# Performance work log

Measured on AMD Instinct MI355X. Metric: run time of the kernel, lower is better.

## Reference

```python
import jax, jax.numpy as jnp
import numpy as np

B, N, D, H, HD, FF, E, V, HID = 32, 125, 256, 8, 32, 1024, 5, 32000, 128
S = N + 3
MAXPOS = 512
EPS = 1e-12       # BERT LayerNorm eps
THRESH = 0.7


def setup_inputs() -> dict:
    key = jax.random.key(0)
    ks = iter(jax.random.split(key, 32))
    def rn(shape):
        return jax.random.normal(next(ks), shape, jnp.float32)
    def p(shape):
        return rn(shape) * 0.02
    inp = {
        "h_t": rn((B, D)),
        "e_task": rn((B, D)),
        "e_layout": rn((B, D)),
        "token_embeds": rn((B, N, D)),
        # router: Linear(768,128) -> ReLU -> Linear(128,5)
        "router_W1": p((3 * D, HID)), "router_b1": jnp.zeros((HID,), jnp.float32),
        "router_W2": p((HID, E)), "router_b2": jnp.zeros((E,), jnp.float32),
        "hint_W": p((D, E)), "hint_b": jnp.zeros((E,), jnp.float32),
        # per-expert BERT params, stacked over expert dim E
        "pos_emb": p((E, MAXPOS, D)),
        "type_emb": p((E, D)),                    # token_type_id=0 row only
        "ln_emb_g": jnp.ones((E, D), jnp.float32), "ln_emb_b": jnp.zeros((E, D), jnp.float32),
        "Wq": p((E, D, D)), "bq": jnp.zeros((E, D), jnp.float32),
        "Wk": p((E, D, D)), "bk": jnp.zeros((E, D), jnp.float32),
        "Wv": p((E, D, D)), "bv": jnp.zeros((E, D), jnp.float32),
        "Wo": p((E, D, D)), "bo": jnp.zeros((E, D), jnp.float32),
        "ln_attn_g": jnp.ones((E, D), jnp.float32), "ln_attn_b": jnp.zeros((E, D), jnp.float32),
        "Wf1": p((E, D, FF)), "bf1": jnp.zeros((E, FF), jnp.float32),
        "Wf2": p((E, FF, D)), "bf2": jnp.zeros((E, D), jnp.float32),
        "ln_ffn_g": jnp.ones((E, D), jnp.float32), "ln_ffn_b": jnp.zeros((E, D), jnp.float32),
        "head_W": p((D, V)), "head_b": jnp.zeros((V,), jnp.float32),
        "top_k": 2,
    }
    return inp


def _ln(x, g, b):
    m = jnp.mean(x, axis=-1, keepdims=True)
    v = jnp.mean(jnp.square(x - m), axis=-1, keepdims=True)
    return (x - m) * jax.lax.rsqrt(v + EPS) * g + b


def _expert(pos, typ, g0, b0, Wq, bq, Wk, bk, Wv, bv, Wo, bo, g1, b1,
            Wf1, bf1, Wf2, bf2, g2, b2, x):
    # 1-layer BERT encoder (eval mode, no causal mask for inputs_embeds).
    Bx, Sx, _ = x.shape
    h = _ln(x + pos[:Sx][None] + typ[None, None], g0, b0)        # [B,S,D]
    q = (h @ Wq + bq).reshape(Bx, Sx, H, HD)
    k = (h @ Wk + bk).reshape(Bx, Sx, H, HD)
    v = (h @ Wv + bv).reshape(Bx, Sx, H, HD)
    scores = jnp.einsum("bqhd,bkhd->bhqk", q, k) / np.float32(np.sqrt(HD))
    attn = jax.nn.softmax(scores, axis=-1)
    ctx = jnp.einsum("bhqk,bkhd->bqhd", attn, v).reshape(Bx, Sx, D)
    h = _ln(h + ctx @ Wo + bo, g1, b1)
    f = jax.nn.gelu(h @ Wf1 + bf1, approximate=False)
    h = _ln(h + f @ Wf2 + bf2, g2, b2)
    return h


def reference(h_t, e_task, e_layout, token_embeds,
              router_W1, router_b1, router_W2, router_b2, hint_W, hint_b,
              pos_emb, type_emb, ln_emb_g, ln_emb_b,
              Wq, bq, Wk, bk, Wv, bv, Wo, bo, ln_attn_g, ln_attn_b,
              Wf1, bf1, Wf2, bf2, ln_ffn_g, ln_ffn_b,
              head_W, head_b, top_k):
    prefix = jnp.stack([h_t, e_task, e_layout], axis=1)            # [B,3,D]
    x_t = jnp.concatenate([prefix, token_embeds], axis=1)          # [B,S,D]
    flat = jnp.concatenate([h_t, e_task, e_layout], axis=-1)       # [B,3D]
    gate_logits = (jax.nn.relu(flat @ router_W1 + router_b1) @ router_W2
                   + router_b2 + e_layout @ hint_W + hint_b)
    gate_probs = jax.nn.softmax(gate_logits, axis=-1)              # [B,E]
    topk_vals, topk_idx = jax.lax.top_k(gate_probs, top_k)         # [B,k]
    # k collapses to 1 only if EVERY row's max prob exceeds threshold
    use_k1 = jnp.all(jnp.max(gate_probs, axis=-1) > THRESH)
    keep = jnp.where(jnp.arange(top_k) == 0, 1.0,
                     jnp.where(use_k1, 0.0, 1.0)).astype(gate_probs.dtype)
    w = topk_vals * keep[None, :]                                  # [B,k]
    # run all experts densely (E=5 small), then gated combine
    expert_outs = jax.vmap(_expert, in_axes=(0,) * 20 + (None,))(
        pos_emb, type_emb, ln_emb_g, ln_emb_b,
        Wq, bq, Wk, bk, Wv, bv, Wo, bo, ln_attn_g, ln_attn_b,
        Wf1, bf1, Wf2, bf2, ln_ffn_g, ln_ffn_b, x_t)               # [E,B,S,D]
    onehot = jax.nn.one_hot(topk_idx, E, dtype=w.dtype)            # [B,k,E]
    comb = jnp.einsum("bk,bke->be", w, onehot)                     # [B,E]
    z = jnp.einsum("be,ebsd->bsd", comb, expert_outs)              # [B,S,D]
    logits = z @ head_W + head_b                                   # [B,S,V]
    return logits, gate_probs
```

## Files before the change

### kernel.cpp

```cpp
#include <hip/hip_runtime.h>
#include <hip/hip_bf16.h>
#include <math.h>

namespace {

constexpr int B = 32, N = 125, D = 256, H = 8, HD = 32, FF = 1024,
              E = 5, V = 32000, HID = 128, S = 128, MAXPOS = 512;
constexpr int BSD = B * S * D;
constexpr float EPS = 1e-12f;
constexpr float THRESH = 0.7f;

constexpr size_t GW_Q = 0, GW_K = 65536, GW_V = 131072, GW_O = 196608,
                 GW_F1 = 262144, GW_F2 = 524288, GW_STRIDE = 786432;

typedef __attribute__((ext_vector_type(4))) float f32x4;
typedef __attribute__((ext_vector_type(8))) short short8v;

__device__ __forceinline__ short f2bf(float f) {
  __hip_bfloat16 h = __float2bfloat16(f);
  short s;
  __builtin_memcpy(&s, &h, 2);
  return s;
}

__device__ __forceinline__ float gelu_exact(float x) {
  return 0.5f * x * (1.f + erff(x * 0.70710678118654752f));
}

__device__ __forceinline__ float wave_sum64(float v) {
#pragma unroll
  for (int off = 32; off > 0; off >>= 1) v += __shfl_xor(v, off);
  return v;
}

__device__ __forceinline__ void gload16(const void* g, void* l) {
  __builtin_amdgcn_global_load_lds(
      (const __attribute__((address_space(1))) unsigned int*)g,
      (__attribute__((address_space(3))) unsigned int*)l, 16, 0, 0);
}

__global__ __launch_bounds__(HID) void router1_kernel(
    const float* __restrict__ h_t, const float* __restrict__ e_task,
    const float* __restrict__ e_layout, const float* __restrict__ W1,
    const float* __restrict__ b1, const float* __restrict__ W2,
    const float* __restrict__ b2, const float* __restrict__ hintW,
    const float* __restrict__ hintb, float* __restrict__ gp_ws,
    float* __restrict__ gp_out) {
  int b = blockIdx.x;
  int t = threadIdx.x;
  float acc = b1[t];
  const float* rows[3] = {h_t + b * D, e_task + b * D, e_layout + b * D};
  for (int seg = 0; seg < 3; ++seg) {
    const float* r = rows[seg];
    const float* w = W1 + (size_t)seg * D * HID;
    for (int i = 0; i < D; ++i) acc += r[i] * w[i * HID + t];
  }
  __shared__ float hid[HID];
  __shared__ float logits[E];
  hid[t] = fmaxf(acc, 0.f);
  __syncthreads();
  if (t < E) {
    float l = b2[t] + hintb[t];
    for (int hh = 0; hh < HID; ++hh) l += hid[hh] * W2[hh * E + t];
    const float* el = e_layout + b * D;
    for (int dd = 0; dd < D; ++dd) l += el[dd] * hintW[dd * E + t];
    logits[t] = l;
  }
  __syncthreads();
  if (t == 0) {
    float mx = logits[0];
    for (int e2 = 1; e2 < E; ++e2) mx = fmaxf(mx, logits[e2]);
    float p[E];
    float se = 0.f;
    for (int e2 = 0; e2 < E; ++e2) {
      p[e2] = expf(logits[e2] - mx);
      se += p[e2];
    }
    float inv = 1.f / se;
    for (int e2 = 0; e2 < E; ++e2) {
      float pe = p[e2] * inv;
      gp_ws[b * E + e2] = pe;
      gp_out[b * E + e2] = pe;
    }
  }
}

__global__ __launch_bounds__(64) void router2_kernel(
    const float* __restrict__ gp, const int* __restrict__ topk_ptr,
    float* __restrict__ comb) {
  __shared__ int allk1;
  int t = threadIdx.x;
  if (t == 0) allk1 = 1;
  __syncthreads();
  float p[E];
  if (t < B) {
    float mx = 0.f;
    for (int e2 = 0; e2 < E; ++e2) {
      p[e2] = gp[t * E + e2];
      mx = fmaxf(mx, p[e2]);
    }
    if (!(mx > THRESH)) allk1 = 0;
  }
  __syncthreads();
  int k1 = allk1;
  if (t < B) {
    for (int e2 = 0; e2 < E; ++e2) comb[t * E + e2] = 0.f;
    int tk = *topk_ptr;
    if (tk > E) tk = E;
    float q[E];
    for (int e2 = 0; e2 < E; ++e2) q[e2] = p[e2];
    for (int kk = 0; kk < tk; ++kk) {
      int bi = 0;
      float bv = q[0];
      for (int e2 = 1; e2 < E; ++e2)
        if (q[e2] > bv) { bv = q[e2]; bi = e2; }
      float w = (kk == 0) ? bv : (k1 ? 0.f : bv);
      comb[t * E + bi] += w;
      q[bi] = -1.f;
    }
  }
}

__device__ __forceinline__ void prep_body(const float* __restrict__ Wp,
                                          short* __restrict__ Gp, int K,
                                          int Nc) {
  __shared__ float Wl[64][65];
  int t = threadIdx.x;
  int n0 = blockIdx.x * 64, k0 = blockIdx.y * 64;
#pragma unroll
  for (int p = 0; p < 4; ++p) {
    int krow = p * 16 + (t >> 4);
    int nc = (t & 15) * 4;
    float4 v = *reinterpret_cast<const float4*>(
        Wp + (size_t)(k0 + krow) * Nc + n0 + nc);
    Wl[krow][nc] = v.x; Wl[krow][nc + 1] = v.y;
    Wl[krow][nc + 2] = v.z; Wl[krow][nc + 3] = v.w;
  }
  __syncthreads();
#pragma unroll
  for (int p = 0; p < 2; ++p) {
    int gid = p * 256 + t;
    int nl = gid >> 3, kg = gid & 7;
    int xv = (nl >> 1) & 3;
    int bk = kg >> 2, s = kg & 3;
    int sp = s ^ xv;
    short8v o;
#pragma unroll
    for (int j = 0; j < 8; ++j) o[j] = f2bf(Wl[kg * 8 + j][nl]);
    *reinterpret_cast<short8v*>(
        Gp + (size_t)(n0 + nl) * K + ((k0 >> 5) + bk) * 32 + sp * 8) = o;
  }
}

__global__ __launch_bounds__(256) void prep_w(
    const float* __restrict__ W, short* __restrict__ G, int K, int Nc,
    size_t estrW, size_t estrG) {
  int e = blockIdx.z;
  prep_body(W + (size_t)e * estrW, G + (size_t)e * estrG, K, Nc);
}

__global__ __launch_bounds__(256) void prep_qkvo(
    const float* __restrict__ Wq, const float* __restrict__ Wk,
    const float* __restrict__ Wv, const float* __restrict__ Wo,
    short* __restrict__ Gw) {
  int z = blockIdx.z;
  int e = z >> 2, which = z & 3;
  const float* W =
      (which == 0 ? Wq : which == 1 ? Wk : which == 2 ? Wv : Wo) +
      (size_t)e * 65536;
  short* G = Gw + (size_t)e * GW_STRIDE + (size_t)which * 65536;
  prep_body(W, G, 256, 256);
}

__global__ __launch_bounds__(256) void embed_ln_w(
    const float* __restrict__ h_t, const float* __restrict__ e_task,
    const float* __restrict__ e_layout, const float* __restrict__ tok,
    const float* __restrict__ pos_b, const float* __restrict__ typ_b,
    const float* __restrict__ g_b, const float* __restrict__ bb_b,
    float* __restrict__ out_b, const float* __restrict__ comb) {
  int e = blockIdx.y;
  int t = threadIdx.x, lane = t & 63, w = t >> 6;
  int row = blockIdx.x * 4 + w;
  int b = row >> 7, s = row & 127;
  if (comb[b * E + e] == 0.f) return;
  const float* pos_e = pos_b + (size_t)e * MAXPOS * D;
  const float* typ_e = typ_b + (size_t)e * D;
  const float* g = g_b + (size_t)e * D;
  const float* bb = bb_b + (size_t)e * D;
  float* outp = out_b + (size_t)e * BSD;
  int d0 = lane * 4;
  const float* src = (s >= 3) ? tok + ((size_t)(b * N + s - 3)) * D
                   : (s == 0) ? h_t + (size_t)b * D
                   : (s == 1) ? e_task + (size_t)b * D
                              : e_layout + (size_t)b * D;
  float4 x = *reinterpret_cast<const float4*>(src + d0);
  float4 pe = *reinterpret_cast<const float4*>(pos_e + (size_t)s * D + d0);
  float4 te = *reinterpret_cast<const float4*>(typ_e + d0);
  x.x += pe.x + te.x; x.y += pe.y + te.y;
  x.z += pe.z + te.z; x.w += pe.w + te.w;
  float mean = wave_sum64(x.x + x.y + x.z + x.w) * (1.f / D);
  float4 xm = {x.x - mean, x.y - mean, x.z - mean, x.w - mean};
  float vv = wave_sum64(xm.x * xm.x + xm.y * xm.y + xm.z * xm.z + xm.w * xm.w);
  float rs = rsqrtf(vv * (1.f / D) + EPS);
  float4 g4 = *reinterpret_cast<const float4*>(g + d0);
  float4 b4 = *reinterpret_cast<const float4*>(bb + d0);
  float4 o = {xm.x * rs * g4.x + b4.x, xm.y * rs * g4.y + b4.y,
              xm.z * rs * g4.z + b4.z, xm.w * rs * g4.w + b4.w};
  *reinterpret_cast<float4*>(outp + (size_t)row * D + d0) = o;
}

__global__ __launch_bounds__(256) void add_ln_w(
    const float* __restrict__ A_b, const float* __restrict__ R_b,
    const float* __restrict__ g_b, const float* __restrict__ bb_b,
    float* __restrict__ out_b, const float* __restrict__ comb) {
  int e = blockIdx.y;
  int t = threadIdx.x, lane = t & 63, w = t >> 6;
  int row = blockIdx.x * 4 + w;
  int b = row >> 7;
  if (comb[b * E + e] == 0.f) return;
  const float* A = A_b + (size_t)e * BSD;
  const float* R = R_b + (size_t)e * BSD;
  const float* g = g_b + (size_t)e * D;
  const float* bb = bb_b + (size_t)e * D;
  float* outp = out_b + (size_t)e * BSD;
  int d0 = lane * 4;
  float4 a4 = *reinterpret_cast<const float4*>(A + (size_t)row * D + d0);
  float4 r4 = *reinterpret_cast<const float4*>(R + (size_t)row * D + d0);
  float4 x = {a4.x + r4.x, a4.y + r4.y, a4.z + r4.z, a4.w + r4.w};
  float mean = wave_sum64(x.x + x.y + x.z + x.w) * (1.f / D);
  float4 xm = {x.x - mean, x.y - mean, x.z - mean, x.w - mean};
  float vv = wave_sum64(xm.x * xm.x + xm.y * xm.y + xm.z * xm.z + xm.w * xm.w);
  float rs = rsqrtf(vv * (1.f / D) + EPS);
  float4 g4 = *reinterpret_cast<const float4*>(g + d0);
  float4 b4 = *reinterpret_cast<const float4*>(bb + d0);
  float4 o = {xm.x * rs * g4.x + b4.x, xm.y * rs * g4.y + b4.y,
              xm.z * rs * g4.z + b4.z, xm.w * rs * g4.w + b4.w};
  *reinterpret_cast<float4*>(outp + (size_t)row * D + d0) = o;
}

template <int BF16>
__global__ __launch_bounds__(256) void ln2_combine(
    const float* __restrict__ A_b, const float* __restrict__ R_b,
    const float* __restrict__ g_b, const float* __restrict__ bb_b,
    const float* __restrict__ comb, short* __restrict__ zs,
    float* __restrict__ zf) {
  int t = threadIdx.x, lane = t & 63, w = t >> 6;
  int row = blockIdx.x * 4 + w;
  int b = row >> 7;
  int d0 = lane * 4;
  float4 z4 = {0.f, 0.f, 0.f, 0.f};
  for (int e = 0; e < E; ++e) {
    float c = comb[b * E + e];
    if (c == 0.f) continue;
    const float* A = A_b + (size_t)e * BSD + (size_t)row * D;
    const float* R = R_b + (size_t)e * BSD + (size_t)row * D;
    float4 a4 = *reinterpret_cast<const float4*>(A + d0);
    float4 r4 = *reinterpret_cast<const float4*>(R + d0);
    float4 x = {a4.x + r4.x, a4.y + r4.y, a4.z + r4.z, a4.w + r4.w};
    float mean = wave_sum64(x.x + x.y + x.z + x.w) * (1.f / D);
    float4 xm = {x.x - mean, x.y - mean, x.z - mean, x.w - mean};
    float vv =
        wave_sum64(xm.x * xm.x + xm.y * xm.y + xm.z * xm.z + xm.w * xm.w);
    float rs = rsqrtf(vv * (1.f / D) + EPS);
    float4 g4 = *reinterpret_cast<const float4*>(g_b + (size_t)e * D + d0);
    float4 b4 = *reinterpret_cast<const float4*>(bb_b + (size_t)e * D + d0);
    z4.x += c * (xm.x * rs * g4.x + b4.x);
    z4.y += c * (xm.y * rs * g4.y + b4.y);
    z4.z += c * (xm.z * rs * g4.z + b4.z);
    z4.w += c * (xm.w * rs * g4.w + b4.w);
  }
  if (BF16) {
    int col = d0;
    int xv = (row >> 1) & 3;
    int colp = (col & ~24) | ((((col >> 3) & 3) ^ xv) << 3);
    short4 o;
    o.x = f2bf(z4.x); o.y = f2bf(z4.y); o.z = f2bf(z4.z); o.w = f2bf(z4.w);
    *reinterpret_cast<short4*>(zs + (size_t)row * 256 + colp) = o;
  } else {
    *reinterpret_cast<float4*>(zf + (size_t)row * D + d0) = z4;
  }
}

__global__ __launch_bounds__(128) void attn2_kernel(
    const float* __restrict__ Qb, const float* __restrict__ Kb,
    const float* __restrict__ Vb, float* __restrict__ Cb,
    const float* __restrict__ comb) {
  int e = blockIdx.y;
  int bh = blockIdx.x;
  int b = bh >> 3, h = bh & 7;
  if (comb[b * E + e] == 0.f) return;
  const float* Q = Qb + (size_t)e * BSD;
  const float* K = Kb + (size_t)e * BSD;
  const float* Vv = Vb + (size_t)e * BSD;
  float* C = Cb + (size_t)e * BSD;
  __shared__ float Ks[S][36];
  __shared__ float Vs[S][36];
  int t = threadIdx.x;
  const float* kb = K + ((size_t)(b * S + t)) * D + h * HD;
  const float* vb = Vv + ((size_t)(b * S + t)) * D + h * HD;
#pragma unroll
  for (int d = 0; d < HD; d += 4) {
    *reinterpret_cast<float4*>(&Ks[t][d]) =
        *reinterpret_cast<const float4*>(kb + d);
    *reinterpret_cast<float4*>(&Vs[t][d]) =
        *reinterpret_cast<const float4*>(vb + d);
  }
  float4 qv[8];
  const float* qp = Q + ((size_t)(b * S + t)) * D + h * HD;
#pragma unroll
  for (int j = 0; j < 8; ++j)
    qv[j] = *reinterpret_cast<const float4*>(qp + j * 4);
  __syncthreads();
  const float scale = 0.17677669529663687f;
  float mx = -1e30f;
  for (int k = 0; k < S; ++k) {
    float s = 0.f;
#pragma unroll
    for (int j = 0; j < 8; ++j) {
      float4 k4 = *reinterpret_cast<const float4*>(&Ks[k][j * 4]);
      s += qv[j].x * k4.x + qv[j].y * k4.y + qv[j].z * k4.z + qv[j].w * k4.w;
    }
    mx = fmaxf(mx, s * scale);
  }
  float se = 0.f;
  float4 cx[8];
#pragma unroll
  for (int j = 0; j < 8; ++j) cx[j] = {0.f, 0.f, 0.f, 0.f};
  for (int k = 0; k < S; ++k) {
    float s = 0.f;
#pragma unroll
    for (int j = 0; j < 8; ++j) {
      float4 k4 = *reinterpret_cast<const float4*>(&Ks[k][j * 4]);
      s += qv[j].x * k4.x + qv[j].y * k4.y + qv[j].z * k4.z + qv[j].w * k4.w;
    }
    float p = expf(s * scale - mx);
    se += p;
#pragma unroll
    for (int j = 0; j < 8; ++j) {
      float4 v4 = *reinterpret_cast<const float4*>(&Vs[k][j * 4]);
      cx[j].x += p * v4.x; cx[j].y += p * v4.y;
      cx[j].z += p * v4.z; cx[j].w += p * v4.w;
    }
  }
  float inv = 1.f / se;
  float* cp = C + ((size_t)(b * S + t)) * D + h * HD;
#pragma unroll
  for (int j = 0; j < 8; ++j) {
    float4 o = {cx[j].x * inv, cx[j].y * inv, cx[j].z * inv, cx[j].w * inv};
    *reinterpret_cast<float4*>(cp + j * 4) = o;
  }
}

template <int ACT, int K, int Nc, int ABF16, int OBF16>
__device__ __forceinline__ void gemm2_body(
    const char* __restrict__ Ag, const short* __restrict__ Gg,
    const float* __restrict__ bias, char* __restrict__ outp, int row0,
    int col0) {
  __shared__ short Al[128 * 40];
  __shared__ short Bl[128 * 32];
  const int t = threadIdx.x;
  const int lane = t & 63;
  const int w = t >> 6;
  const int wr = w >> 1, wc = w & 1;
  const int lrow = lane & 15;
  const int g = lane >> 4;
  const int lkoff = g * 8;
  const int koff = (g ^ ((lrow >> 1) & 3)) << 3;
  const char* Gb = (const char*)Gg;
  char* Bb = (char*)Bl;
  const int srow = t >> 2, sgrp = t & 3;
  const int woff = w * 1024;

  f32x4 acc[4][4];
#pragma unroll
  for (int m = 0; m < 4; ++m)
#pragma unroll
    for (int n = 0; n < 4; ++n) acc[m][n] = (f32x4){0.f, 0.f, 0.f, 0.f};

  for (int k0 = 0; k0 < K; k0 += 32) {
#pragma unroll
    for (int i = 0; i < 2; ++i) {
      int row = i * 64 + srow;
      gload16(Gb + (size_t)(col0 + row) * (K * 2) + (k0 >> 5) * 64 + sgrp * 16,
              Bb + i * 4096 + woff);
    }
    if (ABF16) {
      int row = t >> 1, c0 = (t & 1) * 2;
#pragma unroll
      for (int c = 0; c < 2; ++c) {
        short8v v = *reinterpret_cast<const short8v*>(
            (const short*)Ag + (size_t)(row0 + row) * K + k0 + (c0 + c) * 8);
        *reinterpret_cast<short8v*>(&Al[row * 40 + (c0 + c) * 8]) = v;
      }
    } else {
#pragma unroll
      for (int j = 0; j < 4; ++j) {
        int id = t + 256 * j;
        int row = id >> 3, s4 = id & 7;
        float4 a4 = *reinterpret_cast<const float4*>(
            (const float*)Ag + (size_t)(row0 + row) * K + k0 + s4 * 4);
        short4 p;
        p.x = f2bf(a4.x); p.y = f2bf(a4.y); p.z = f2bf(a4.z); p.w = f2bf(a4.w);
        *reinterpret_cast<short4*>(&Al[row * 40 + s4 * 4]) = p;
      }
    }
    __syncthreads();
    short8v af[4], bfv[4];
#pragma unroll
    for (int m = 0; m < 4; ++m)
      af[m] = *reinterpret_cast<const short8v*>(
          &Al[(wr * 64 + m * 16 + lrow) * 40 + lkoff]);
#pragma unroll
    for (int n = 0; n < 4; ++n)
      bfv[n] = *reinterpret_cast<const short8v*>(
          &Bl[(wc * 64 + n * 16 + lrow) * 32 + koff]);
#pragma unroll
    for (int m = 0; m < 4; ++m)
#pragma unroll
      for (int n = 0; n < 4; ++n)
        acc[m][n] = __builtin_amdgcn_mfma_f32_16x16x32_bf16(
            af[m], bfv[n], acc[m][n], 0, 0, 0);
    __syncthreads();
  }
#pragma unroll
  for (int n = 0; n < 4; ++n) {
    int col = col0 + wc * 64 + n * 16 + lrow;
    float bc = bias[col];
#pragma unroll
    for (int m = 0; m < 4; ++m) {
      int rbase = row0 + wr * 64 + m * 16 + g * 4;
      f32x4 v = acc[m][n];
#pragma unroll
      for (int r = 0; r < 4; ++r) {
        float o = v[r] + bc;
        if (ACT == 1) o = gelu_exact(o);
        if (OBF16)
          ((short*)outp)[(size_t)(rbase + r) * Nc + col] = f2bf(o);
        else
          ((float*)outp)[(size_t)(rbase + r) * Nc + col] = o;
      }
    }
  }
}

template <int ACT, int K, int Nc, int ABF16, int OBF16>
__device__ __forceinline__ void gemm2_body64(
    const char* __restrict__ Ag, const short* __restrict__ Gg,
    const float* __restrict__ bias, char* __restrict__ outp, int row0,
    int col0) {
  __shared__ short Al[64 * 40];
  __shared__ short Bl[128 * 32];
  const int t = threadIdx.x;
  const int lane = t & 63;
  const int w = t >> 6;
  const int lrow = lane & 15;
  const int g = lane >> 4;
  const int lkoff = g * 8;
  const int koff = (g ^ ((lrow >> 1) & 3)) << 3;
  const char* Gb = (const char*)Gg;
  char* Bb = (char*)Bl;
  const int srow = t >> 2, sgrp = t & 3;
  const int woff = w * 1024;

  f32x4 acc[4][2];
#pragma unroll
  for (int m = 0; m < 4; ++m)
#pragma unroll
    for (int n = 0; n < 2; ++n) acc[m][n] = (f32x4){0.f, 0.f, 0.f, 0.f};

  for (int k0 = 0; k0 < K; k0 += 32) {
#pragma unroll
    for (int i = 0; i < 2; ++i) {
      int row = i * 64 + srow;
      gload16(Gb + (size_t)(col0 + row) * (K * 2) + (k0 >> 5) * 64 + sgrp * 16,
              Bb + i * 4096 + woff);
    }
    if (ABF16) {
      int row = t >> 2, seg = t & 3;
      short8v v = *reinterpret_cast<const short8v*>(
          (const short*)Ag + (size_t)(row0 + row) * K + k0 + seg * 8);
      *reinterpret_cast<short8v*>(&Al[row * 40 + seg * 8]) = v;
    } else {
#pragma unroll
      for (int j = 0; j < 2; ++j) {
        int id = t + 256 * j;
        int row = id >> 3, s4 = id & 7;
        float4 a4 = *reinterpret_cast<const float4*>(
            (const float*)Ag + (size_t)(row0 + row) * K + k0 + s4 * 4);
        short4 p;
        p.x = f2bf(a4.x); p.y = f2bf(a4.y); p.z = f2bf(a4.z); p.w = f2bf(a4.w);
        *reinterpret_cast<short4*>(&Al[row * 40 + s4 * 4]) = p;
      }
    }
    __syncthreads();
    short8v af[4], bfv[2];
#pragma unroll
    for (int m = 0; m < 4; ++m)
      af[m] = *reinterpret_cast<const short8v*>(
          &Al[(m * 16 + lrow) * 40 + lkoff]);
#pragma unroll
    for (int n = 0; n < 2; ++n)
      bfv[n] = *reinterpret_cast<const short8v*>(
          &Bl[(w * 32 + n * 16 + lrow) * 32 + koff]);
#pragma unroll
    for (int m = 0; m < 4; ++m)
#pragma unroll
      for (int n = 0; n < 2; ++n)
        acc[m][n] = __builtin_amdgcn_mfma_f32_16x16x32_bf16(
            af[m], bfv[n], acc[m][n], 0, 0, 0);
    __syncthreads();
  }
#pragma unroll
  for (int n = 0; n < 2; ++n) {
    int col = col0 + w * 32 + n * 16 + lrow;
    float bc = bias[col];
#pragma unroll
    for (int m = 0; m < 4; ++m) {
      int rbase = row0 + m * 16 + g * 4;
      f32x4 v = acc[m][n];
#pragma unroll
      for (int r = 0; r < 4; ++r) {
        float o = v[r] + bc;
        if (ACT == 1) o = gelu_exact(o);
        if (OBF16)
          ((short*)outp)[(size_t)(rbase + r) * Nc + col] = f2bf(o);
        else
          ((float*)outp)[(size_t)(rbase + r) * Nc + col] = o;
      }
    }
  }
}

template <int ACT, int K, int Nc, int ABF16, int OBF16>
__global__ __launch_bounds__(256) void gemm2_e(
    const char* __restrict__ Ab, const short* __restrict__ Gbase,
    const float* __restrict__ biasb, char* __restrict__ outb,
    const float* __restrict__ comb, size_t aStrB, size_t oStrB, int bStr) {
  int e = blockIdx.z;
  int row0 = blockIdx.y * 128;
  int col0 = blockIdx.x * 128;
  if (comb[(row0 >> 7) * E + e] == 0.f) return;
  gemm2_body<ACT, K, Nc, ABF16, OBF16>(
      Ab + (size_t)e * aStrB, Gbase + (size_t)e * GW_STRIDE,
      biasb + (size_t)e * bStr, outb + (size_t)e * oStrB, row0, col0);
}

template <int ACT, int K, int Nc, int ABF16, int OBF16>
__global__ __launch_bounds__(256) void gemm2b64_e(
    const char* __restrict__ Ab, const short* __restrict__ Gbase,
    const float* __restrict__ biasb, char* __restrict__ outb,
    const float* __restrict__ comb, size_t aStrB, size_t oStrB, int bStr) {
  int e = blockIdx.z;
  int row0 = blockIdx.y * 64;
  int col0 = blockIdx.x * 128;
  if (comb[(row0 >> 7) * E + e] == 0.f) return;
  gemm2_body64<ACT, K, Nc, ABF16, OBF16>(
      Ab + (size_t)e * aStrB, Gbase + (size_t)e * GW_STRIDE,
      biasb + (size_t)e * bStr, outb + (size_t)e * oStrB, row0, col0);
}

__global__ __launch_bounds__(256) void qkv2_e(
    const float* __restrict__ h0b, const short* __restrict__ Gw,
    const float* __restrict__ bqb, const float* __restrict__ bkb,
    const float* __restrict__ bvb, float* __restrict__ qb,
    float* __restrict__ kb, float* __restrict__ vb,
    const float* __restrict__ comb) {
  int e = blockIdx.z;
  int which = blockIdx.x >> 1;
  int col0 = (blockIdx.x & 1) * 128;
  int row0 = blockIdx.y * 128;
  if (comb[(row0 >> 7) * E + e] == 0.f) return;
  const short* G = Gw + (size_t)e * GW_STRIDE + (size_t)which * 65536;
  const float* bias =
      (which == 0 ? bqb : which == 1 ? bkb : bvb) + (size_t)e * D;
  float* outp = (which == 0 ? qb : which == 1 ? kb : vb) + (size_t)e * BSD;
  gemm2_body<0, D, D, 0, 0>((const char*)h0b + (size_t)e * BSD * 4, G, bias,
                            (char*)outp, row0, col0);
}

template <int ACT, int K, int Nc>
__device__ __forceinline__ void gemm_body(
    const float* __restrict__ Ag, const float* __restrict__ Wg,
    const float* __restrict__ bias, float* __restrict__ outp, int row0,
    int col0) {
  __shared__ short Al[128 * 40];
  __shared__ short Bl[128 * 40];
  const int t = threadIdx.x;
  const int lane = t & 63;
  const int w = t >> 6;
  const int wr = w >> 1, wc = w & 1;
  const int lrow = lane & 15;
  const int lkoff = (lane >> 4) * 8;
  f32x4 acc[4][4];
#pragma unroll
  for (int m = 0; m < 4; ++m)
#pragma unroll
    for (int n = 0; n < 4; ++n) acc[m][n] = (f32x4){0.f, 0.f, 0.f, 0.f};
  const int colB = t >> 1, kh = (t & 1) * 16;
  for (int k0 = 0; k0 < K; k0 += 32) {
#pragma unroll
    for (int j = 0; j < 4; ++j) {
      int id = t + 256 * j;
      int row = id >> 3, s4 = id & 7;
      float4 a4 = *reinterpret_cast<const float4*>(
          Ag + (size_t)(row0 + row) * K + k0 + s4 * 4);
      short4 p;
      p.x = f2bf(a4.x); p.y = f2bf(a4.y); p.z = f2bf(a4.z); p.w = f2bf(a4.w);
      *reinterpret_cast<short4*>(&Al[row * 40 + s4 * 4]) = p;
    }
    {
      const float* wp = Wg + (size_t)(k0 + kh) * Nc + (col0 + colB);
      short8v v0, v1;
#pragma unroll
      for (int kk = 0; kk < 8; ++kk) v0[kk] = f2bf(wp[(size_t)kk * Nc]);
#pragma unroll
      for (int kk = 0; kk < 8; ++kk) v1[kk] = f2bf(wp[(size_t)(kk + 8) * Nc]);
      *reinterpret_cast<short8v*>(&Bl[colB * 40 + kh]) = v0;
      *reinterpret_cast<short8v*>(&Bl[colB * 40 + kh + 8]) = v1;
    }
    __syncthreads();
    short8v af[4], bfv[4];
#pragma unroll
    for (int m = 0; m < 4; ++m)
      af[m] = *reinterpret_cast<const short8v*>(
          &Al[(wr * 64 + m * 16 + lrow) * 40 + lkoff]);
#pragma unroll
    for (int n = 0; n < 4; ++n)
      bfv[n] = *reinterpret_cast<const short8v*>(
          &Bl[(wc * 64 + n * 16 + lrow) * 40 + lkoff]);
#pragma unroll
    for (int m = 0; m < 4; ++m)
#pragma unroll
      for (int n = 0; n < 4; ++n)
        acc[m][n] = __builtin_amdgcn_mfma_f32_16x16x32_bf16(
            af[m], bfv[n], acc[m][n], 0, 0, 0);
    __syncthreads();
  }
#pragma unroll
  for (int n = 0; n < 4; ++n) {
    int col = col0 + wc * 64 + n * 16 + lrow;
    float bc = bias[col];
#pragma unroll
    for (int m = 0; m < 4; ++m) {
      int rbase = row0 + wr * 64 + m * 16 + (lane >> 4) * 4;
      f32x4 v = acc[m][n];
#pragma unroll
      for (int r = 0; r < 4; ++r) {
        float o = v[r] + bc;
        if (ACT == 1) o = gelu_exact(o);
        outp[(size_t)(rbase + r) * Nc + col] = o;
      }
    }
  }
}

__global__ __launch_bounds__(256) void head_gemm(
    const float* __restrict__ Ag, const float* __restrict__ Wg,
    const float* __restrict__ bias, float* __restrict__ outp) {
  int row0 = blockIdx.x * 128;
  int col0 = blockIdx.y * 128;
  gemm_body<0, D, V>(Ag, Wg, bias, outp, row0, col0);
}

__global__ __launch_bounds__(256) void head_gemm2(
    const short* __restrict__ zs, const short* __restrict__ G,
    const float* __restrict__ bias, float* __restrict__ outp) {
  __shared__ short Al[128 * 32];
  __shared__ short Bl[128 * 32];
  const int row0 = blockIdx.x * 128;
  const int col0 = blockIdx.y * 128;
  const int t = threadIdx.x;
  const int lane = t & 63, w = t >> 6;
  const int wr = w >> 1, wc = w & 1;
  const int lrow = lane & 15;
  const int g = lane >> 4;
  const int koff = (g ^ ((lrow >> 1) & 3)) << 3;
  const int srow = t >> 2, sgrp = t & 3;
  const char* zsb = (const char*)zs;
  const char* Gb = (const char*)G;
  char* Ab = (char*)Al;
  char* Bb = (char*)Bl;
  const int woff = w * 1024;

  f32x4 acc[4][4];
#pragma unroll
  for (int m = 0; m < 4; ++m)
#pragma unroll
    for (int n = 0; n < 4; ++n) acc[m][n] = (f32x4){0.f, 0.f, 0.f, 0.f};

  for (int kb = 0; kb < 8; ++kb) {
#pragma unroll
    for (int i = 0; i < 2; ++i) {
      int row = i * 64 + srow;
      gload16(zsb + (size_t)(row0 + row) * 512 + kb * 64 + sgrp * 16,
              Ab + i * 4096 + woff);
      gload16(Gb + (size_t)(col0 + row) * 512 + kb * 64 + sgrp * 16,
              Bb + i * 4096 + woff);
    }
    __syncthreads();
    short8v af[4], bfv[4];
#pragma unroll
    for (int m = 0; m < 4; ++m)
      af[m] = *reinterpret_cast<const short8v*>(
          &Al[(wr * 64 + m * 16 + lrow) * 32 + koff]);
#pragma unroll
    for (int n = 0; n < 4; ++n)
      bfv[n] = *reinterpret_cast<const short8v*>(
          &Bl[(wc * 64 + n * 16 + lrow) * 32 + koff]);
#pragma unroll
    for (int m = 0; m < 4; ++m)
#pragma unroll
      for (int n = 0; n < 4; ++n)
        acc[m][n] = __builtin_amdgcn_mfma_f32_16x16x32_bf16(
            af[m], bfv[n], acc[m][n], 0, 0, 0);
    __syncthreads();
  }
#pragma unroll
  for (int n = 0; n < 4; ++n) {
    int col = col0 + wc * 64 + n * 16 + lrow;
    float bc = bias[col];
#pragma unroll
    for (int m = 0; m < 4; ++m) {
      int rbase = row0 + wr * 64 + m * 16 + g * 4;
      f32x4 v = acc[m][n];
#pragma unroll
      for (int r = 0; r < 4; ++r)
        outp[(size_t)(rbase + r) * V + col] = v[r] + bc;
    }
  }
}

__global__ __launch_bounds__(256) void combine_f32(
    const float* __restrict__ hb, const float* __restrict__ comb,
    float* __restrict__ zf) {
  size_t i = ((size_t)blockIdx.x * 256 + threadIdx.x) * 4;
  int b = (int)(i >> 15);
  float4 acc = {0.f, 0.f, 0.f, 0.f};
#pragma unroll
  for (int e2 = 0; e2 < E; ++e2) {
    float c = comb[b * E + e2];
    if (c != 0.f) {
      float4 v = *reinterpret_cast<const float4*>(hb + (size_t)e2 * BSD + i);
      acc.x += c * v.x; acc.y += c * v.y;
      acc.z += c * v.z; acc.w += c * v.w;
    }
  }
  *reinterpret_cast<float4*>(zf + i) = acc;
}

}

extern "C" void kernel_launch(void* const* d_in, const int* in_sizes, int n_in,
                              void* d_out, int out_size, void* d_ws,
                              size_t ws_size, hipStream_t stream) {
  const float* h_t = (const float*)d_in[0];
  const float* e_task = (const float*)d_in[1];
  const float* e_layout = (const float*)d_in[2];
  const float* tok = (const float*)d_in[3];
  const float* rW1 = (const float*)d_in[4];
  const float* rb1 = (const float*)d_in[5];
  const float* rW2 = (const float*)d_in[6];
  const float* rb2 = (const float*)d_in[7];
  const float* hW = (const float*)d_in[8];
  const float* hb = (const float*)d_in[9];
  const float* pos = (const float*)d_in[10];
  const float* typ = (const float*)d_in[11];
  const float* g0 = (const float*)d_in[12];
  const float* b0 = (const float*)d_in[13];
  const float* Wq = (const float*)d_in[14];
  const float* bq = (const float*)d_in[15];
  const float* Wk = (const float*)d_in[16];
  const float* bk = (const float*)d_in[17];
  const float* Wv = (const float*)d_in[18];
  const float* bv = (const float*)d_in[19];
  const float* Wo = (const float*)d_in[20];
  const float* bo = (const float*)d_in[21];
  const float* g1 = (const float*)d_in[22];
  const float* b1 = (const float*)d_in[23];
  const float* Wf1 = (const float*)d_in[24];
  const float* bf1 = (const float*)d_in[25];
  const float* Wf2 = (const float*)d_in[26];
  const float* bf2 = (const float*)d_in[27];
  const float* g2 = (const float*)d_in[28];
  const float* b2 = (const float*)d_in[29];
  const float* headW = (const float*)d_in[30];
  const float* headb = (const float*)d_in[31];
  const int* topk = (const int*)d_in[32];

  float* out = (float*)d_out;
  float* gp_out = out + (size_t)B * S * V;

  float* h0 = out;
  float* qb2 = h0 + (size_t)E * BSD;
  float* kb2 = qb2 + (size_t)E * BSD;
  float* vb2 = kb2 + (size_t)E * BSD;
  float* ctxb = vb2 + (size_t)E * BSD;
  short* fbh = (short*)(ctxb + (size_t)E * BSD);
  short* Gw = (short*)(out + (size_t)25 * BSD + 10485760);

  float* wsf = (float*)d_ws;
  short* Ghead = (short*)d_ws;
  float* comb = wsf + 4096000;
  float* gp = comb + 256;
  short* zs = (short*)(wsf + 4096512);
  size_t need = (size_t)4096512 * 4 + (size_t)4096 * 256 * 2;
  bool fast_head = ws_size >= need;
  if (!fast_head) {
    comb = wsf;
    gp = comb + 256;
  }
  float* zf = gp + 256;

  if (fast_head)
    prep_w<<<dim3(V / 64, 4, 1), 256, 0, stream>>>(headW, Ghead, 256, V, 0, 0);
  prep_qkvo<<<dim3(4, 4, E * 4), 256, 0, stream>>>(Wq, Wk, Wv, Wo, Gw);
  prep_w<<<dim3(16, 4, E), 256, 0, stream>>>(Wf1, Gw + GW_F1, 256, 1024,
                                             262144, GW_STRIDE);
  prep_w<<<dim3(4, 16, E), 256, 0, stream>>>(Wf2, Gw + GW_F2, 1024, 256,
                                             262144, GW_STRIDE);

  router1_kernel<<<B, HID, 0, stream>>>(h_t, e_task, e_layout, rW1, rb1, rW2,
                                        rb2, hW, hb, gp, gp_out);
  router2_kernel<<<1, 64, 0, stream>>>(gp, topk, comb);

  dim3 gLN(B * S / 4, E);
  embed_ln_w<<<gLN, 256, 0, stream>>>(h_t, e_task, e_layout, tok, pos, typ,
                                      g0, b0, h0, comb);
  qkv2_e<<<dim3(6, 32, E), 256, 0, stream>>>(h0, Gw, bq, bk, bv, qb2, kb2,
                                             vb2, comb);
  attn2_kernel<<<dim3(B * H, E), 128, 0, stream>>>(qb2, kb2, vb2, ctxb, comb);
  gemm2b64_e<0, 256, 256, 0, 0><<<dim3(2, 64, E), 256, 0, stream>>>(
      (const char*)ctxb, Gw + GW_O, bo, (char*)qb2, comb, (size_t)BSD * 4,
      (size_t)BSD * 4, 256);
  add_ln_w<<<gLN, 256, 0, stream>>>(h0, qb2, g1, b1, kb2, comb);
  gemm2_e<1, 256, 1024, 0, 1><<<dim3(8, 32, E), 256, 0, stream>>>(
      (const char*)kb2, Gw + GW_F1, bf1, (char*)fbh, comb, (size_t)BSD * 4,
      (size_t)B * S * FF * 2, FF);
  gemm2b64_e<0, 1024, 256, 1, 0><<<dim3(2, 64, E), 256, 0, stream>>>(
      (const char*)fbh, Gw + GW_F2, bf2, (char*)vb2, comb,
      (size_t)B * S * FF * 2, (size_t)BSD * 4, 256);

  if (fast_head) {
    ln2_combine<1><<<B * S / 4, 256, 0, stream>>>(kb2, vb2, g2, b2, comb, zs,
                                                  nullptr);
    head_gemm2<<<dim3(32, V / 128), 256, 0, stream>>>(zs, Ghead, headb, out);
  } else {
    add_ln_w<<<gLN, 256, 0, stream>>>(kb2, vb2, g2, b2, h0, comb);
    combine_f32<<<BSD / 1024, 256, 0, stream>>>(h0, comb, zf);
    head_gemm<<<dim3(32, V / 128), 256, 0, stream>>>(zf, headW, headb, out);
  }
  (void)in_sizes; (void)n_in; (void)out_size;
}
```

Baseline: 434.5 us.

## Store all intermediate expert activations in bf16 instead of fp32

Switches the per-expert intermediate buffers (embedding LN output, Q/K/V, attention context, attention output, LN1 output, FFN output) from fp32 to bf16. GEMM kernels now take bf16 inputs and write bf16 outputs, and the LN and attention kernels convert on load and store. This roughly halves the memory traffic between stages and lets the GEMMs skip an fp32-to-bf16 conversion on load. In exchange it adds rounding error to residual paths and LayerNorm inputs.

After: 404.0 us. 1.08x faster.

```diff
diff --git a/kernel.cpp b/kernel.cpp
--- a/kernel.cpp
+++ b/kernel.cpp
@@ -7,6 +7,7 @@
 constexpr int B = 32, N = 125, D = 256, H = 8, HD = 32, FF = 1024,
               E = 5, V = 32000, HID = 128, S = 128, MAXPOS = 512;
 constexpr int BSD = B * S * D;
+constexpr int BSF = B * S * FF;
 constexpr float EPS = 1e-12f;
 constexpr float THRESH = 0.7f;
 
@@ -21,6 +22,13 @@
   short s;
   __builtin_memcpy(&s, &h, 2);
   return s;
+}
+
+__device__ __forceinline__ float bf2f(short s) {
+  unsigned int u = ((unsigned int)(unsigned short)s) << 16;
+  float f;
+  __builtin_memcpy(&f, &u, 4);
+  return f;
 }
 
 __device__ __forceinline__ float gelu_exact(float x) {
@@ -177,7 +185,7 @@
     const float* __restrict__ e_layout, const float* __restrict__ tok,
     const float* __restrict__ pos_b, const float* __restrict__ typ_b,
     const float* __restrict__ g_b, const float* __restrict__ bb_b,
-    float* __restrict__ out_b, const float* __restrict__ comb) {
+    short* __restrict__ out_b, const float* __restrict__ comb) {
   int e = blockIdx.y;
   int t = threadIdx.x, lane = t & 63, w = t >> 6;
   int row = blockIdx.x * 4 + w;
@@ -187,7 +195,7 @@
   const float* typ_e = typ_b + (size_t)e * D;
   const float* g = g_b + (size_t)e * D;
   const float* bb = bb_b + (size_t)e * D;
-  float* outp = out_b + (size_t)e * BSD;
+  short* outp = out_b + (size_t)e * BSD;
   int d0 = lane * 4;
   const float* src = (s >= 3) ? tok + ((size_t)(b * N + s - 3)) * D
                    : (s == 0) ? h_t + (size_t)b * D
@@ -204,43 +212,50 @@
   float rs = rsqrtf(vv * (1.f / D) + EPS);
   float4 g4 = *reinterpret_cast<const float4*>(g + d0);
   float4 b4 = *reinterpret_cast<const float4*>(bb + d0);
-  float4 o = {xm.x * rs * g4.x + b4.x, xm.y * rs * g4.y + b4.y,
-              xm.z * rs * g4.z + b4.z, xm.w * rs * g4.w + b4.w};
-  *reinterpret_cast<float4*>(outp + (size_t)row * D + d0) = o;
+  short4 o;
+  o.x = f2bf(xm.x * rs * g4.x + b4.x);
+  o.y = f2bf(xm.y * rs * g4.y + b4.y);
+  o.z = f2bf(xm.z * rs * g4.z + b4.z);
+  o.w = f2bf(xm.w * rs * g4.w + b4.w);
+  *reinterpret_cast<short4*>(outp + (size_t)row * D + d0) = o;
 }
 
 __global__ __launch_bounds__(256) void add_ln_w(
-    const float* __restrict__ A_b, const float* __restrict__ R_b,
+    const short* __restrict__ A_b, const short* __restrict__ R_b,
     const float* __restrict__ g_b, const float* __restrict__ bb_b,
-    float* __restrict__ out_b, const float* __restrict__ comb) {
+    short* __restrict__ out_b, const float* __restrict__ comb) {
   int e = blockIdx.y;
   int t = threadIdx.x, lane = t & 63, w = t >> 6;
   int row = blockIdx.x * 4 + w;
   int b = row >> 7;
   if (comb[b * E + e] == 0.f) return;
-  const float* A = A_b + (size_t)e * BSD;
-  const float* R = R_b + (size_t)e * BSD;
+  const short* A = A_b + (size_t)e * BSD + (size_t)row * D;
+  const short* R = R_b + (size_t)e * BSD + (size_t)row * D;
   const float* g = g_b + (size_t)e * D;
   const float* bb = bb_b + (size_t)e * D;
-  float* outp = out_b + (size_t)e * BSD;
+  short* outp = out_b + (size_t)e * BSD;
   int d0 = lane * 4;
-  float4 a4 = *reinterpret_cast<const float4*>(A + (size_t)row * D + d0);
-  float4 r4 = *reinterpret_cast<const float4*>(R + (size_t)row * D + d0);
-  float4 x = {a4.x + r4.x, a4.y + r4.y, a4.z + r4.z, a4.w + r4.w};
+  short4 a4 = *reinterpret_cast<const short4*>(A + d0);
+  short4 r4 = *reinterpret_cast<const short4*>(R + d0);
+  float4 x = {bf2f(a4.x) + bf2f(r4.x), bf2f(a4.y) + bf2f(r4.y),
+              bf2f(a4.z) + bf2f(r4.z), bf2f(a4.w) + bf2f(r4.w)};
   float mean = wave_sum64(x.x + x.y + x.z + x.w) * (1.f / D);
   float4 xm = {x.x - mean, x.y - mean, x.z - mean, x.w - mean};
   float vv = wave_sum64(xm.x * xm.x + xm.y * xm.y + xm.z * xm.z + xm.w * xm.w);
   float rs = rsqrtf(vv * (1.f / D) + EPS);
   float4 g4 = *reinterpret_cast<const float4*>(g + d0);
   float4 b4 = *reinterpret_cast<const float4*>(bb + d0);
-  float4 o = {xm.x * rs * g4.x + b4.x, xm.y * rs * g4.y + b4.y,
-              xm.z * rs * g4.z + b4.z, xm.w * rs * g4.w + b4.w};
-  *reinterpret_cast<float4*>(outp + (size_t)row * D + d0) = o;
+  short4 o;
+  o.x = f2bf(xm.x * rs * g4.x + b4.x);
+  o.y = f2bf(xm.y * rs * g4.y + b4.y);
+  o.z = f2bf(xm.z * rs * g4.z + b4.z);
+  o.w = f2bf(xm.w * rs * g4.w + b4.w);
+  *reinterpret_cast<short4*>(outp + (size_t)row * D + d0) = o;
 }
 
 template <int BF16>
 __global__ __launch_bounds__(256) void ln2_combine(
-    const float* __restrict__ A_b, const float* __restrict__ R_b,
+    const short* __restrict__ A_b, const short* __restrict__ R_b,
     const float* __restrict__ g_b, const float* __restrict__ bb_b,
     const float* __restrict__ comb, short* __restrict__ zs,
     float* __restrict__ zf) {
@@ -252,11 +267,12 @@
   for (int e = 0; e < E; ++e) {
     float c = comb[b * E + e];
     if (c == 0.f) continue;
-    const float* A = A_b + (size_t)e * BSD + (size_t)row * D;
-    const float* R = R_b + (size_t)e * BSD + (size_t)row * D;
-    float4 a4 = *reinterpret_cast<const float4*>(A + d0);
-    float4 r4 = *reinterpret_cast<const float4*>(R + d0);
-    float4 x = {a4.x + r4.x, a4.y + r4.y, a4.z + r4.z, a4.w + r4.w};
+    const short* A = A_b + (size_t)e * BSD + (size_t)row * D;
+    const short* R = R_b + (size_t)e * BSD + (size_t)row * D;
+    short4 a4 = *reinterpret_cast<const short4*>(A + d0);
+    short4 r4 = *reinterpret_cast<const short4*>(R + d0);
+    float4 x = {bf2f(a4.x) + bf2f(r4.x), bf2f(a4.y) + bf2f(r4.y),
+                bf2f(a4.z) + bf2f(r4.z), bf2f(a4.w) + bf2f(r4.w)};
     float mean = wave_sum64(x.x + x.y + x.z + x.w) * (1.f / D);
     float4 xm = {x.x - mean, x.y - mean, x.z - mean, x.w - mean};
     float vv =
@@ -282,34 +298,41 @@
 }
 
 __global__ __launch_bounds__(128) void attn2_kernel(
-    const float* __restrict__ Qb, const float* __restrict__ Kb,
-    const float* __restrict__ Vb, float* __restrict__ Cb,
+    const short* __restrict__ Qb, const short* __restrict__ Kb,
+    const short* __restrict__ Vb, short* __restrict__ Cb,
     const float* __restrict__ comb) {
   int e = blockIdx.y;
   int bh = blockIdx.x;
   int b = bh >> 3, h = bh & 7;
   if (comb[b * E + e] == 0.f) return;
-  const float* Q = Qb + (size_t)e * BSD;
-  const float* K = Kb + (size_t)e * BSD;
-  const float* Vv = Vb + (size_t)e * BSD;
-  float* C = Cb + (size_t)e * BSD;
+  const short* Q = Qb + (size_t)e * BSD;
+  const short* K = Kb + (size_t)e * BSD;
+  const short* Vv = Vb + (size_t)e * BSD;
+  short* C = Cb + (size_t)e * BSD;
   __shared__ float Ks[S][36];
   __shared__ float Vs[S][36];
   int t = threadIdx.x;
-  const float* kb = K + ((size_t)(b * S + t)) * D + h * HD;
-  const float* vb = Vv + ((size_t)(b * S + t)) * D + h * HD;
-#pragma unroll
-  for (int d = 0; d < HD; d += 4) {
-    *reinterpret_cast<float4*>(&Ks[t][d]) =
-        *reinterpret_cast<const float4*>(kb + d);
-    *reinterpret_cast<float4*>(&Vs[t][d]) =
-        *reinterpret_cast<const float4*>(vb + d);
+  const short* kbp = K + ((size_t)(b * S + t)) * D + h * HD;
+  const short* vbp = Vv + ((size_t)(b * S + t)) * D + h * HD;
+#pragma unroll
+  for (int j = 0; j < 4; ++j) {
+    short8v k8 = *reinterpret_cast<const short8v*>(kbp + j * 8);
+    short8v v8 = *reinterpret_cast<const short8v*>(vbp + j * 8);
+#pragma unroll
+    for (int c = 0; c < 8; ++c) {
+      Ks[t][j * 8 + c] = bf2f(k8[c]);
+      Vs[t][j * 8 + c] = bf2f(v8[c]);
+    }
   }
   float4 qv[8];
-  const float* qp = Q + ((size_t)(b * S + t)) * D + h * HD;
-#pragma unroll
-  for (int j = 0; j < 8; ++j)
-    qv[j] = *reinterpret_cast<const float4*>(qp + j * 4);
+  const short* qp = Q + ((size_t)(b * S + t)) * D + h * HD;
+#pragma unroll
+  for (int j = 0; j < 4; ++j) {
+    short8v q8 = *reinterpret_cast<const short8v*>(qp + j * 8);
+    qv[j * 2] = (float4){bf2f(q8[0]), bf2f(q8[1]), bf2f(q8[2]), bf2f(q8[3])};
+    qv[j * 2 + 1] =
+        (float4){bf2f(q8[4]), bf2f(q8[5]), bf2f(q8[6]), bf2f(q8[7])};
+  }
   __syncthreads();
   const float scale = 0.17677669529663687f;
   float mx = -1e30f;
@@ -325,7 +348,7 @@
   float se = 0.f;
   float4 cx[8];
 #pragma unroll
-  for (int j = 0; j < 8; ++j) cx[j] = {0.f, 0.f, 0.f, 0.f};
+  for (int j = 0; j < 8; ++j) cx[j] = (float4){0.f, 0.f, 0.f, 0.f};
   for (int k = 0; k < S; ++k) {
     float s = 0.f;
 #pragma unroll
@@ -343,11 +366,13 @@
     }
   }
   float inv = 1.f / se;
-  float* cp = C + ((size_t)(b * S + t)) * D + h * HD;
+  short* cp = C + ((size_t)(b * S + t)) * D + h * HD;
 #pragma unroll
   for (int j = 0; j < 8; ++j) {
-    float4 o = {cx[j].x * inv, cx[j].y * inv, cx[j].z * inv, cx[j].w * inv};
-    *reinterpret_cast<float4*>(cp + j * 4) = o;
+    short4 o;
+    o.x = f2bf(cx[j].x * inv); o.y = f2bf(cx[j].y * inv);
+    o.z = f2bf(cx[j].z * inv); o.w = f2bf(cx[j].w * inv);
+    *reinterpret_cast<short4*>(cp + j * 4) = o;
   }
 }
 
@@ -560,10 +585,10 @@
 }
 
 __global__ __launch_bounds__(256) void qkv2_e(
-    const float* __restrict__ h0b, const short* __restrict__ Gw,
+    const short* __restrict__ h0b, const short* __restrict__ Gw,
     const float* __restrict__ bqb, const float* __restrict__ bkb,
-    const float* __restrict__ bvb, float* __restrict__ qb,
-    float* __restrict__ kb, float* __restrict__ vb,
+    const float* __restrict__ bvb, short* __restrict__ qb,
+    short* __restrict__ kb, short* __restrict__ vb,
     const float* __restrict__ comb) {
   int e = blockIdx.z;
   int which = blockIdx.x >> 1;
@@ -573,8 +598,8 @@
   const short* G = Gw + (size_t)e * GW_STRIDE + (size_t)which * 65536;
   const float* bias =
       (which == 0 ? bqb : which == 1 ? bkb : bvb) + (size_t)e * D;
-  float* outp = (which == 0 ? qb : which == 1 ? kb : vb) + (size_t)e * BSD;
-  gemm2_body<0, D, D, 0, 0>((const char*)h0b + (size_t)e * BSD * 4, G, bias,
+  short* outp = (which == 0 ? qb : which == 1 ? kb : vb) + (size_t)e * BSD;
+  gemm2_body<0, D, D, 1, 1>((const char*)(h0b + (size_t)e * BSD), G, bias,
                             (char*)outp, row0, col0);
 }
 
@@ -731,7 +756,7 @@
 }
 
 __global__ __launch_bounds__(256) void combine_f32(
-    const float* __restrict__ hb, const float* __restrict__ comb,
+    const short* __restrict__ hb, const float* __restrict__ comb,
     float* __restrict__ zf) {
   size_t i = ((size_t)blockIdx.x * 256 + threadIdx.x) * 4;
   int b = (int)(i >> 15);
@@ -740,9 +765,9 @@
   for (int e2 = 0; e2 < E; ++e2) {
     float c = comb[b * E + e2];
     if (c != 0.f) {
-      float4 v = *reinterpret_cast<const float4*>(hb + (size_t)e2 * BSD + i);
-      acc.x += c * v.x; acc.y += c * v.y;
-      acc.z += c * v.z; acc.w += c * v.w;
+      short4 v = *reinterpret_cast<const short4*>(hb + (size_t)e2 * BSD + i);
+      acc.x += c * bf2f(v.x); acc.y += c * bf2f(v.y);
+      acc.z += c * bf2f(v.z); acc.w += c * bf2f(v.w);
     }
   }
   *reinterpret_cast<float4*>(zf + i) = acc;
@@ -790,13 +815,13 @@
   float* out = (float*)d_out;
   float* gp_out = out + (size_t)B * S * V;
 
-  float* h0 = out;
-  float* qb2 = h0 + (size_t)E * BSD;
-  float* kb2 = qb2 + (size_t)E * BSD;
-  float* vb2 = kb2 + (size_t)E * BSD;
-  float* ctxb = vb2 + (size_t)E * BSD;
-  short* fbh = (short*)(ctxb + (size_t)E * BSD);
-  short* Gw = (short*)(out + (size_t)25 * BSD + 10485760);
+  short* h0s = (short*)out;
+  short* qs = h0s + (size_t)E * BSD;
+  short* ks = qs + (size_t)E * BSD;
+  short* vs = ks + (size_t)E * BSD;
+  short* ctxs = vs + (size_t)E * BSD;
+  short* fbh = ctxs + (size_t)E * BSD;
+  short* Gw = fbh + (size_t)E * BSF;
 
   float* wsf = (float*)d_ws;
   short* Ghead = (short*)d_ws;
@@ -825,28 +850,28 @@
 
   dim3 gLN(B * S / 4, E);
   embed_ln_w<<<gLN, 256, 0, stream>>>(h_t, e_task, e_layout, tok, pos, typ,
-                                      g0, b0, h0, comb);
-  qkv2_e<<<dim3(6, 32, E), 256, 0, stream>>>(h0, Gw, bq, bk, bv, qb2, kb2,
-                                             vb2, comb);
-  attn2_kernel<<<dim3(B * H, E), 128, 0, stream>>>(qb2, kb2, vb2, ctxb, comb);
-  gemm2b64_e<0, 256, 256, 0, 0><<<dim3(2, 64, E), 256, 0, stream>>>(
-      (const char*)ctxb, Gw + GW_O, bo, (char*)qb2, comb, (size_t)BSD * 4,
-      (size_t)BSD * 4, 256);
-  add_ln_w<<<gLN, 256, 0, stream>>>(h0, qb2, g1, b1, kb2, comb);
-  gemm2_e<1, 256, 1024, 0, 1><<<dim3(8, 32, E), 256, 0, stream>>>(
-      (const char*)kb2, Gw + GW_F1, bf1, (char*)fbh, comb, (size_t)BSD * 4,
-      (size_t)B * S * FF * 2, FF);
-  gemm2b64_e<0, 1024, 256, 1, 0><<<dim3(2, 64, E), 256, 0, stream>>>(
-      (const char*)fbh, Gw + GW_F2, bf2, (char*)vb2, comb,
-      (size_t)B * S * FF * 2, (size_t)BSD * 4, 256);
+                                      g0, b0, h0s, comb);
+  qkv2_e<<<dim3(6, 32, E), 256, 0, stream>>>(h0s, Gw, bq, bk, bv, qs, ks, vs,
+                                             comb);
+  attn2_kernel<<<dim3(B * H, E), 128, 0, stream>>>(qs, ks, vs, ctxs, comb);
+  gemm2b64_e<0, 256, 256, 1, 1><<<dim3(2, 64, E), 256, 0, stream>>>(
+      (const char*)ctxs, Gw + GW_O, bo, (char*)qs, comb, (size_t)BSD * 2,
+      (size_t)BSD * 2, 256);
+  add_ln_w<<<gLN, 256, 0, stream>>>(h0s, qs, g1, b1, ks, comb);
+  gemm2_e<1, 256, 1024, 1, 1><<<dim3(8, 32, E), 256, 0, stream>>>(
+      (const char*)ks, Gw + GW_F1, bf1, (char*)fbh, comb, (size_t)BSD * 2,
+      (size_t)BSF * 2, FF);
+  gemm2b64_e<0, 1024, 256, 1, 1><<<dim3(2, 64, E), 256, 0, stream>>>(
+      (const char*)fbh, Gw + GW_F2, bf2, (char*)vs, comb, (size_t)BSF * 2,
+      (size_t)BSD * 2, 256);
 
   if (fast_head) {
-    ln2_combine<1><<<B * S / 4, 256, 0, stream>>>(kb2, vb2, g2, b2, comb, zs,
+    ln2_combine<1><<<B * S / 4, 256, 0, stream>>>(ks, vs, g2, b2, comb, zs,
                                                   nullptr);
     head_gemm2<<<dim3(32, V / 128), 256, 0, stream>>>(zs, Ghead, headb, out);
   } else {
-    add_ln_w<<<gLN, 256, 0, stream>>>(kb2, vb2, g2, b2, h0, comb);
-    combine_f32<<<BSD / 1024, 256, 0, stream>>>(h0, comb, zf);
+    add_ln_w<<<gLN, 256, 0, stream>>>(ks, vs, g2, b2, h0s, comb);
+    combine_f32<<<BSD / 1024, 256, 0, stream>>>(h0s, comb, zf);
     head_gemm<<<dim3(32, V / 128), 256, 0, stream>>>(zf, headW, headb, out);
   }
   (void)in_sizes; (void)n_in; (void)out_size;
```
